# Kernel optimization log

Measured on AMD Instinct MI355X. Metric: run time of the kernel, lower is better.

## Reference

```python
import jax, jax.numpy as jnp
import numpy as np

B, C, D, H, W = 4, 128, 16, 16, 16
HID = 128
EPS = 1e-5


def setup_inputs() -> dict:
    key = jax.random.key(0)
    ks = jax.random.split(key, 10)
    s = 1.0 / np.sqrt(C)
    return {
        "x": jax.random.normal(ks[0], (B, C, D, H, W), dtype=jnp.float32),
        "Wq": jax.random.normal(ks[1], (HID, C), dtype=jnp.float32) * s,
        "bq": jax.random.normal(ks[2], (HID,), dtype=jnp.float32) * s,
        "Wk": jax.random.normal(ks[3], (HID, C), dtype=jnp.float32) * s,
        "bk": jax.random.normal(ks[4], (HID,), dtype=jnp.float32) * s,
        "Wv": jax.random.normal(ks[5], (HID, C), dtype=jnp.float32) * s,
        "bv": jax.random.normal(ks[6], (HID,), dtype=jnp.float32) * s,
        "bn_weight": jax.random.normal(ks[7], (HID,), dtype=jnp.float32),
        "bn_bias": jax.random.normal(ks[8], (HID,), dtype=jnp.float32),
        "gamma": jax.random.normal(ks[9], (1,), dtype=jnp.float32),
    }


def reference(x, Wq, bq, Wk, bk, Wv, bv, bn_weight, bn_bias, gamma):
    b, c, d, h, w = x.shape
    n = d * h * w
    xf = x.reshape(b, c, n)  # [B, C, N]
    # 1x1 conv3d == per-voxel linear: [B, hid, N]
    q = jnp.einsum("hc,bcn->bnh", Wq, xf) + bq  # [B, N, hid] (query permuted)
    k = jnp.einsum("hc,bcn->bhn", Wk, xf) + bk[None, :, None]  # [B, hid, N]
    v = jnp.einsum("hc,bcn->bhn", Wv, xf) + bv[None, :, None]  # [B, hid, N]
    # unscaled attention scores [B, N, N], softmax over last dim
    attn = jax.nn.softmax(jnp.einsum("bih,bhj->bij", q, k), axis=-1)
    # out[b,h,i] = sum_j v[b,h,j] * attn[b,i,j]
    out = jnp.einsum("bhj,bij->bhi", v, attn)  # [B, hid, N]
    # BatchNorm3d (training mode): per-channel stats over (B, N), biased var
    mean = jnp.mean(out, axis=(0, 2), keepdims=True)
    var = jnp.mean(jnp.square(out - mean), axis=(0, 2), keepdims=True)
    out = (out - mean) * jax.lax.rsqrt(var + EPS)
    out = out * bn_weight[None, :, None] + bn_bias[None, :, None]
    out = gamma[0] * out.reshape(b, c, d, h, w) + x
    return out
```

## Files before the change

### kernel.cpp

```cpp
#include <hip/hip_runtime.h>


#define NV 4096
#define LOG2E 1.44269504088896340736f
#define EPSV 1e-5f

typedef float f32x4 __attribute__((ext_vector_type(4)));
typedef short bf16x8 __attribute__((ext_vector_type(8)));
typedef unsigned short u16x4 __attribute__((ext_vector_type(4)));
typedef unsigned short u16x8 __attribute__((ext_vector_type(8)));
typedef unsigned int u32x2 __attribute__((ext_vector_type(2)));

static __device__ __forceinline__ unsigned short f2bf(float f) {
    union { float f; unsigned u; } v; v.f = f;
    unsigned r = v.u + 0x7FFFu + ((v.u >> 16) & 1u);
    return (unsigned short)(r >> 16);
}
static __device__ __forceinline__ float bf2f(unsigned short u) {
    union { unsigned u; float f; } v; v.u = ((unsigned)u) << 16; return v.f;
}
static __device__ __forceinline__ unsigned fbits(float f) {
    union { float f; unsigned u; } v; v.f = f; return v.u;
}

__global__ __launch_bounds__(256) void projx_kernel(
    const float* __restrict__ x,
    const float* __restrict__ Wq, const float* __restrict__ Wk,
    const float* __restrict__ Wv,
    const float* __restrict__ bq, const float* __restrict__ bk,
    const float* __restrict__ bv,
    unsigned short* __restrict__ Qb, unsigned short* __restrict__ Kb,
    unsigned short* __restrict__ Vb)
{
    __shared__ unsigned short xt[64 * 136];
    __shared__ unsigned short Wl[128 * 136];
    const int bid = blockIdx.x;
    const int m = bid >> 8, b = (bid >> 6) & 3, n0 = (bid & 63) << 6;
    const int t = threadIdx.x, w = t >> 6, lane = t & 63;
    const int quad = lane >> 4, l16 = lane & 15;

    const float* Wm = (m == 0) ? Wq : ((m == 1) ? Wk : Wv);
    const float* bias = (m == 0) ? bq : ((m == 1) ? bk : bv);

    #pragma unroll
    for (int it = 0; it < 32; ++it) {
        const int e = it * 256 + t;
        const int c = e >> 6, il = e & 63;
        xt[il * 136 + c] = f2bf(x[(((b << 7) + c) << 12) + n0 + il]);
    }
    #pragma unroll
    for (int it = 0; it < 16; ++it) {
        const int idx = it * 1024 + (t << 2);
        const float4 wv4 = *(const float4*)(Wm + idx);
        const int h = idx >> 7, c = idx & 127;
        u16x4 pk;
        pk[0] = f2bf(wv4.x); pk[1] = f2bf(wv4.y);
        pk[2] = f2bf(wv4.z); pk[3] = f2bf(wv4.w);
        *(u16x4*)(Wl + h * 136 + c) = pk;
    }
    __syncthreads();

    bf16x8 af[4];
    {
        const int il = (w << 4) + l16;
        #pragma unroll
        for (int ck = 0; ck < 4; ++ck)
            af[ck] = *(const bf16x8*)(xt + il * 136 + (ck << 5) + (quad << 3));
    }
    if (m == 2) __syncthreads();

    #pragma unroll
    for (int s = 0; s < 8; ++s) {
        const int h = (s << 4) + l16;
        f32x4 acc = {0.f, 0.f, 0.f, 0.f};
        #pragma unroll
        for (int ck = 0; ck < 4; ++ck) {
            const bf16x8 wf = *(const bf16x8*)(Wl + h * 136 + (ck << 5) + (quad << 3));
            acc = __builtin_amdgcn_mfma_f32_16x16x32_bf16(af[ck], wf, acc, 0, 0, 0);
        }
        const float bval = bias[h];
        if (m == 2) {
            #pragma unroll
            for (int r = 0; r < 4; ++r)
                xt[h * 66 + (w << 4) + (quad << 2) + r] = f2bf(acc[r] + bval);
        } else {
            #pragma unroll
            for (int r = 0; r < 4; ++r) {
                float val = acc[r] + bval;
                if (m == 0) val *= LOG2E;
                xt[((w << 4) + (quad << 2) + r) * 136 + h] = f2bf(val);
            }
        }
    }
    __syncthreads();
    if (m == 2) {
        #pragma unroll
        for (int it = 0; it < 32; ++it) {
            const int e = it * 256 + t;
            const int h = e >> 6, il = e & 63;
            Vb[(((b << 7) + h) << 12) + n0 + il] = xt[h * 66 + il];
        }
    } else {
        unsigned short* dst = (m == 0) ? Qb : Kb;
        #pragma unroll
        for (int it = 0; it < 4; ++it) {
            const int e = (it << 8) + t;
            const int row = e >> 4, c8 = (e & 15) << 3;
            *(bf16x8*)(dst + (((b << 12) + n0 + row) << 7) + c8) =
                *(const bf16x8*)(xt + row * 136 + c8);
        }
    }
}

template<int NSL>
__global__ __launch_bounds__(256, 2) void flash_kernel(
    const unsigned short* __restrict__ Qb,
    const unsigned short* __restrict__ Kb,
    const unsigned short* __restrict__ Vb,
    unsigned short* __restrict__ Opart, float* __restrict__ lpart,
    unsigned short* __restrict__ Obuf)
{
    __shared__ unsigned short Kt[64 * 128];
    __shared__ unsigned short Vt[128 * 64];
    __shared__ unsigned short pA[4][32 * 72];
    constexpr int NB = (NSL == 6) ? 768 : NSL * 128;
    const int bid = ((blockIdx.x & 7) * (NB >> 3)) + (blockIdx.x >> 3);
    const int sl = bid >> 7, b = (bid >> 5) & 3, ic = bid & 31;
    const int t = threadIdx.x, w = t >> 6, lane = t & 63;
    const int quad = lane >> 4, l16 = lane & 15;
    const int iw = (ic << 7) + (w << 5);

    int T, joff;
    if constexpr (NSL == 6) {
        T = 11 - (sl >= 4);
        joff = sl * 11 - ((sl >= 5) ? 1 : 0);
    } else {
        T = (NV / NSL) >> 6;
        joff = sl * T;
    }
    const int jbase = joff << 6;
    unsigned short* pAw = pA[w];

    const int ktg = t & 15, ktj = t >> 4;
    const int vtg = t & 7,  vth = t >> 3;
    const int kswz = (ktg ^ ktj) << 3;
    const int vswz = (vtg ^ (vth & 7)) << 3;

    bf16x8 qf[2][4];
    #pragma unroll
    for (int half = 0; half < 2; ++half) {
        const unsigned short* qp =
            Qb + (((b << 12) + iw + (half << 4) + l16) << 7) + (quad << 3);
        #pragma unroll
        for (int ck = 0; ck < 4; ++ck) qf[half][ck] = *(const bf16x8*)(qp + (ck << 5));
    }
    f32x4 Oacc[2][8];
    #pragma unroll
    for (int half = 0; half < 2; ++half)
        #pragma unroll
        for (int s = 0; s < 8; ++s) Oacc[half][s] = (f32x4){0.f, 0.f, 0.f, 0.f};
    float lsum0 = 0.f, lsum1 = 0.f;

    const unsigned short* Kbb = Kb + ((long)b << 19);
    const unsigned short* Vbb = Vb + ((long)b << 19);

    bf16x8 sk[4], sv[4];
    #pragma unroll
    for (int r = 0; r < 4; ++r)
        sk[r] = *(const bf16x8*)(Kbb + ((jbase + (r << 4) + ktj) << 7) + (ktg << 3));
    #pragma unroll
    for (int r = 0; r < 4; ++r)
        sv[r] = *(const bf16x8*)(Vbb + (((r << 5) + vth) << 12) + jbase + (vtg << 3));

    for (int t8 = 0; t8 < T; ++t8) {
        const int j0 = jbase + (t8 << 6);

        __syncthreads();
        #pragma unroll
        for (int r = 0; r < 4; ++r)
            *(bf16x8*)(Kt + (((r << 4) + ktj) << 7) + kswz) = sk[r];
        #pragma unroll
        for (int r = 0; r < 4; ++r)
            *(bf16x8*)(Vt + (((r << 5) + vth) << 6) + vswz) = sv[r];
        __syncthreads();

        if (t8 + 1 < T) {
            const int j1 = j0 + 64;
            #pragma unroll
            for (int r = 0; r < 4; ++r)
                sk[r] = *(const bf16x8*)(Kbb + ((j1 + (r << 4) + ktj) << 7) + (ktg << 3));
            #pragma unroll
            for (int r = 0; r < 4; ++r)
                sv[r] = *(const bf16x8*)(Vbb + (((r << 5) + vth) << 12) + j1 + (vtg << 3));
        }

        #pragma unroll
        for (int js = 0; js < 4; ++js) {
            bf16x8 kf[4];
            const int krow = ((js << 4) + l16) << 7;
            #pragma unroll
            for (int ck = 0; ck < 4; ++ck)
                kf[ck] = *(const bf16x8*)(Kt + krow + ((((ck << 2) + quad) ^ l16) << 3));
            f32x4 a0 = {0.f, 0.f, 0.f, 0.f}, a1 = {0.f, 0.f, 0.f, 0.f};
            __builtin_amdgcn_s_setprio(1);
            #pragma unroll
            for (int ck = 0; ck < 4; ++ck) {
                a0 = __builtin_amdgcn_mfma_f32_16x16x32_bf16(kf[ck], qf[0][ck], a0, 0, 0, 0);
                a1 = __builtin_amdgcn_mfma_f32_16x16x32_bf16(kf[ck], qf[1][ck], a1, 0, 0, 0);
            }
            __builtin_amdgcn_s_setprio(0);
            f32x4 e0, e1;
            #pragma unroll
            for (int r = 0; r < 4; ++r) {
                e0[r] = __builtin_amdgcn_exp2f(a0[r]);
                e1[r] = __builtin_amdgcn_exp2f(a1[r]);
            }
            lsum0 += (e0[0] + e0[1]) + (e0[2] + e0[3]);
            lsum1 += (e1[0] + e1[1]) + (e1[2] + e1[3]);
            u32x2 pk0, pk1;
            pk0[0] = __builtin_amdgcn_perm(fbits(e0[1]), fbits(e0[0]), 0x07060302u);
            pk0[1] = __builtin_amdgcn_perm(fbits(e0[3]), fbits(e0[2]), 0x07060302u);
            pk1[0] = __builtin_amdgcn_perm(fbits(e1[1]), fbits(e1[0]), 0x07060302u);
            pk1[1] = __builtin_amdgcn_perm(fbits(e1[3]), fbits(e1[2]), 0x07060302u);
            const int jc = (js << 4) + (quad << 2);
            *(u32x2*)(pAw + l16 * 72 + jc)        = pk0;
            *(u32x2*)(pAw + (16 + l16) * 72 + jc) = pk1;
        }
        bf16x8 pf[2][2];
        #pragma unroll
        for (int half = 0; half < 2; ++half)
            #pragma unroll
            for (int kh = 0; kh < 2; ++kh)
                pf[half][kh] = *(const bf16x8*)(pAw + ((half << 4) + l16) * 72 +
                                                (kh << 5) + (quad << 3));
        #pragma unroll
        for (int s = 0; s < 8; ++s) {
            const int vrow = ((s << 4) + l16) << 6;
            const bf16x8 v0 = *(const bf16x8*)(Vt + vrow + ((quad ^ (l16 & 7)) << 3));
            const bf16x8 v1 = *(const bf16x8*)(Vt + vrow + (((4 + quad) ^ (l16 & 7)) << 3));
            __builtin_amdgcn_s_setprio(1);
            Oacc[0][s] = __builtin_amdgcn_mfma_f32_16x16x32_bf16(v0, pf[0][0], Oacc[0][s], 0, 0, 0);
            Oacc[0][s] = __builtin_amdgcn_mfma_f32_16x16x32_bf16(v1, pf[0][1], Oacc[0][s], 0, 0, 0);
            Oacc[1][s] = __builtin_amdgcn_mfma_f32_16x16x32_bf16(v0, pf[1][0], Oacc[1][s], 0, 0, 0);
            Oacc[1][s] = __builtin_amdgcn_mfma_f32_16x16x32_bf16(v1, pf[1][1], Oacc[1][s], 0, 0, 0);
            __builtin_amdgcn_s_setprio(0);
        }
    }

    float l0 = lsum0; l0 += __shfl_xor(l0, 16); l0 += __shfl_xor(l0, 32);
    float l1 = lsum1; l1 += __shfl_xor(l1, 16); l1 += __shfl_xor(l1, 32);

    if (NSL == 1) {
        const float rl0 = 1.f / l0, rl1 = 1.f / l1;
        #pragma unroll
        for (int s = 0; s < 8; ++s)
            #pragma unroll
            for (int r = 0; r < 4; ++r) {
                const int h = (s << 4) + (quad << 2) + r;
                Obuf[(((b << 7) + h) << 12) + iw + l16]      = f2bf(Oacc[0][s][r] * rl0);
                Obuf[(((b << 7) + h) << 12) + iw + 16 + l16] = f2bf(Oacc[1][s][r] * rl1);
            }
    } else {
        const int slb = (sl << 2) + b;
        if (quad == 0) {
            lpart[(slb << 12) + iw + l16]      = l0;
            lpart[(slb << 12) + iw + 16 + l16] = l1;
        }
        unsigned short* Ob = Opart + ((long)slb << 19);
        #pragma unroll
        for (int half = 0; half < 2; ++half)
            #pragma unroll
            for (int s = 0; s < 8; ++s)
                #pragma unroll
                for (int r = 0; r < 4; ++r) {
                    const int h = (s << 4) + (quad << 2) + r;
                    Ob[(h << 12) + iw + (half << 4) + l16] = f2bf(Oacc[half][s][r]);
                }
    }
}

template<int NSL>
__global__ __launch_bounds__(1024) void mf_kernel(
    const unsigned short* __restrict__ Opart, const float* __restrict__ lpart,
    const float* __restrict__ x, const float* __restrict__ bnw,
    const float* __restrict__ bnb, const float* __restrict__ gammap,
    float* __restrict__ out)
{
    const int h = blockIdx.x;
    const int t = threadIdx.x;
    const int b = t >> 8;
    const int i0 = (t & 255) << 4;

    float A[16], L[16];
    #pragma unroll
    for (int k = 0; k < 16; ++k) { A[k] = 0.f; L[k] = 0.f; }
    #pragma unroll
    for (int sl = 0; sl < NSL; ++sl) {
        const int slb = (sl << 2) + b;
        const u16x8 u0 = *(const u16x8*)(Opart + ((long)slb << 19) + ((long)h << 12) + i0);
        const u16x8 u1 = *(const u16x8*)(Opart + ((long)slb << 19) + ((long)h << 12) + i0 + 8);
        const float* lp = lpart + (slb << 12) + i0;
        #pragma unroll
        for (int k = 0; k < 8; ++k) { A[k] += bf2f(u0[k]); A[8 + k] += bf2f(u1[k]); }
        #pragma unroll
        for (int k = 0; k < 4; ++k) {
            const float4 lv = *(const float4*)(lp + (k << 2));
            L[(k << 2) + 0] += lv.x; L[(k << 2) + 1] += lv.y;
            L[(k << 2) + 2] += lv.z; L[(k << 2) + 3] += lv.w;
        }
    }
    float o[16], s = 0.f, ss = 0.f;
    #pragma unroll
    for (int k = 0; k < 16; ++k) {
        o[k] = A[k] / L[k];
        s += o[k]; ss += o[k] * o[k];
    }
    #pragma unroll
    for (int off = 32; off; off >>= 1) {
        s  += __shfl_down(s, off);
        ss += __shfl_down(ss, off);
    }
    __shared__ float rs[16], rss[16], fin[2];
    const int wid = t >> 6;
    if ((t & 63) == 0) { rs[wid] = s; rss[wid] = ss; }
    __syncthreads();
    if (t == 0) {
        float s2 = 0.f, ss2 = 0.f;
        #pragma unroll
        for (int k = 0; k < 16; ++k) { s2 += rs[k]; ss2 += rss[k]; }
        fin[0] = s2; fin[1] = ss2;
    }
    __syncthreads();
    const float inv = 1.f / 16384.f;
    const float mean = fin[0] * inv;
    const float var  = fin[1] * inv - mean * mean;
    const float g = gammap[0];
    const float scale = bnw[h] * rsqrtf(var + EPSV);
    const float a  = g * scale;
    const float bb = g * (bnb[h] - mean * scale);

    const float* xp = x + (((b << 7) + h) << 12) + i0;
    float* op = out + (((b << 7) + h) << 12) + i0;
    #pragma unroll
    for (int k = 0; k < 4; ++k) {
        const float4 xv = *(const float4*)(xp + (k << 2));
        float4 r;
        r.x = o[(k << 2) + 0] * a + bb + xv.x;
        r.y = o[(k << 2) + 1] * a + bb + xv.y;
        r.z = o[(k << 2) + 2] * a + bb + xv.z;
        r.w = o[(k << 2) + 3] * a + bb + xv.w;
        *(float4*)(op + (k << 2)) = r;
    }
}

__global__ __launch_bounds__(1024) void mf1_kernel(
    const unsigned short* __restrict__ Obuf,
    const float* __restrict__ x, const float* __restrict__ bnw,
    const float* __restrict__ bnb, const float* __restrict__ gammap,
    float* __restrict__ out)
{
    const int h = blockIdx.x;
    const int t = threadIdx.x;
    const int b = t >> 8;
    const int i0 = (t & 255) << 4;
    const u16x8 u0 = *(const u16x8*)(Obuf + (((b << 7) + h) << 12) + i0);
    const u16x8 u1 = *(const u16x8*)(Obuf + (((b << 7) + h) << 12) + i0 + 8);
    float o[16], s = 0.f, ss = 0.f;
    #pragma unroll
    for (int k = 0; k < 8; ++k) { o[k] = bf2f(u0[k]); o[8 + k] = bf2f(u1[k]); }
    #pragma unroll
    for (int k = 0; k < 16; ++k) { s += o[k]; ss += o[k] * o[k]; }
    #pragma unroll
    for (int off = 32; off; off >>= 1) {
        s  += __shfl_down(s, off);
        ss += __shfl_down(ss, off);
    }
    __shared__ float rs[16], rss[16], fin[2];
    const int wid = t >> 6;
    if ((t & 63) == 0) { rs[wid] = s; rss[wid] = ss; }
    __syncthreads();
    if (t == 0) {
        float s2 = 0.f, ss2 = 0.f;
        #pragma unroll
        for (int k = 0; k < 16; ++k) { s2 += rs[k]; ss2 += rss[k]; }
        fin[0] = s2; fin[1] = ss2;
    }
    __syncthreads();
    const float inv = 1.f / 16384.f;
    const float mean = fin[0] * inv;
    const float var  = fin[1] * inv - mean * mean;
    const float g = gammap[0];
    const float scale = bnw[h] * rsqrtf(var + EPSV);
    const float a  = g * scale;
    const float bb = g * (bnb[h] - mean * scale);
    const float* xp = x + (((b << 7) + h) << 12) + i0;
    float* op = out + (((b << 7) + h) << 12) + i0;
    #pragma unroll
    for (int k = 0; k < 4; ++k) {
        const float4 xv = *(const float4*)(xp + (k << 2));
        float4 r;
        r.x = o[(k << 2) + 0] * a + bb + xv.x;
        r.y = o[(k << 2) + 1] * a + bb + xv.y;
        r.z = o[(k << 2) + 2] * a + bb + xv.z;
        r.w = o[(k << 2) + 3] * a + bb + xv.w;
        *(float4*)(op + (k << 2)) = r;
    }
}

extern "C" void kernel_launch(void* const* d_in, const int* in_sizes, int n_in,
                              void* d_out, int out_size, void* d_ws, size_t ws_size,
                              hipStream_t stream) {
    const float* x   = (const float*)d_in[0];
    const float* Wq  = (const float*)d_in[1];
    const float* bq  = (const float*)d_in[2];
    const float* Wk  = (const float*)d_in[3];
    const float* bk  = (const float*)d_in[4];
    const float* Wv  = (const float*)d_in[5];
    const float* bv  = (const float*)d_in[6];
    const float* bnw = (const float*)d_in[7];
    const float* bnb = (const float*)d_in[8];
    const float* gam = (const float*)d_in[9];
    float* out = (float*)d_out;

    char* ws = (char*)d_ws;
    unsigned short* Obuf = (unsigned short*)(ws);
    unsigned short* Qb   = (unsigned short*)(ws + (4u  << 20));
    unsigned short* Kb   = (unsigned short*)(ws + (8u  << 20));
    unsigned short* Vb   = (unsigned short*)(ws + (12u << 20));
    float*          lpart = (float*)(ws + (16u << 20) + (128u << 10));
    unsigned short* Opart = (unsigned short*)(ws + (17u << 20));

    int nsl = 1;
    if      (ws_size >= (17ull << 20) + (32ull << 20)) nsl = 6;
    else if (ws_size >= (17ull << 20) + (16ull << 20)) nsl = 4;
    else if (ws_size >= (17ull << 20) + (8ull  << 20)) nsl = 2;

    projx_kernel<<<768, 256, 0, stream>>>(x, Wq, Wk, Wv, bq, bk, bv, Qb, Kb, Vb);
    if (nsl == 6) {
        flash_kernel<6><<<768, 256, 0, stream>>>(Qb, Kb, Vb, Opart, lpart, Obuf);
        mf_kernel<6><<<128, 1024, 0, stream>>>(Opart, lpart, x, bnw, bnb, gam, out);
    } else if (nsl == 4) {
        flash_kernel<4><<<512, 256, 0, stream>>>(Qb, Kb, Vb, Opart, lpart, Obuf);
        mf_kernel<4><<<128, 1024, 0, stream>>>(Opart, lpart, x, bnw, bnb, gam, out);
    } else if (nsl == 2) {
        flash_kernel<2><<<256, 256, 0, stream>>>(Qb, Kb, Vb, Opart, lpart, Obuf);
        mf_kernel<2><<<128, 1024, 0, stream>>>(Opart, lpart, x, bnw, bnb, gam, out);
    } else {
        flash_kernel<1><<<128, 256, 0, stream>>>(Qb, Kb, Vb, Opart, lpart, Obuf);
        mf1_kernel<<<128, 1024, 0, stream>>>(Obuf, x, bnw, bnb, gam, out);
    }
}
```

Before: 148.3 us.

## Double-buffer K in LDS, stream V fragments from global, vectorize x loads

The flash kernel now double-buffers the K tile in shared memory, so each iteration needs one barrier instead of two. V no longer goes through LDS: each wave reads its MFMA operand fragments directly from global memory with a two-step register prefetch. The setprio hints are removed. The projection kernel loads x with float4 instead of scalar loads. The aim is to cut LDS traffic and barrier stalls, at the cost of redundant global/L2 reads of V across the four waves and more exposed load latency in the PV loop.

```diff
diff --git a/kernel.cpp b/kernel.cpp
--- a/kernel.cpp
+++ b/kernel.cpp
@@ -43,10 +43,14 @@
     const float* bias = (m == 0) ? bq : ((m == 1) ? bk : bv);
 
     #pragma unroll
-    for (int it = 0; it < 32; ++it) {
-        const int e = it * 256 + t;
-        const int c = e >> 6, il = e & 63;
-        xt[il * 136 + c] = f2bf(x[(((b << 7) + c) << 12) + n0 + il]);
+    for (int it = 0; it < 8; ++it) {
+        const int e = (it << 8) + t;
+        const int c = e >> 4, i4 = (e & 15) << 2;
+        const float4 xv = *(const float4*)(x + (((b << 7) + c) << 12) + n0 + i4);
+        xt[(i4 + 0) * 136 + c] = f2bf(xv.x);
+        xt[(i4 + 1) * 136 + c] = f2bf(xv.y);
+        xt[(i4 + 2) * 136 + c] = f2bf(xv.z);
+        xt[(i4 + 3) * 136 + c] = f2bf(xv.w);
     }
     #pragma unroll
     for (int it = 0; it < 16; ++it) {
@@ -120,8 +124,7 @@
     unsigned short* __restrict__ Opart, float* __restrict__ lpart,
     unsigned short* __restrict__ Obuf)
 {
-    __shared__ unsigned short Kt[64 * 128];
-    __shared__ unsigned short Vt[128 * 64];
+    __shared__ unsigned short Kt[2][64 * 128];
     __shared__ unsigned short pA[4][32 * 72];
     constexpr int NB = (NSL == 6) ? 768 : NSL * 128;
     const int bid = ((blockIdx.x & 7) * (NB >> 3)) + (blockIdx.x >> 3);
@@ -142,9 +145,7 @@
     unsigned short* pAw = pA[w];
 
     const int ktg = t & 15, ktj = t >> 4;
-    const int vtg = t & 7,  vth = t >> 3;
     const int kswz = (ktg ^ ktj) << 3;
-    const int vswz = (vtg ^ (vth & 7)) << 3;
 
     bf16x8 qf[2][4];
     #pragma unroll
@@ -163,35 +164,32 @@
 
     const unsigned short* Kbb = Kb + ((long)b << 19);
     const unsigned short* Vbb = Vb + ((long)b << 19);
-
-    bf16x8 sk[4], sv[4];
+    const int vcol = quad << 3;
+
+    bf16x8 sk[4];
     #pragma unroll
     for (int r = 0; r < 4; ++r)
         sk[r] = *(const bf16x8*)(Kbb + ((jbase + (r << 4) + ktj) << 7) + (ktg << 3));
     #pragma unroll
     for (int r = 0; r < 4; ++r)
-        sv[r] = *(const bf16x8*)(Vbb + (((r << 5) + vth) << 12) + jbase + (vtg << 3));
+        *(bf16x8*)(Kt[0] + (((r << 4) + ktj) << 7) + kswz) = sk[r];
+    __syncthreads();
 
     for (int t8 = 0; t8 < T; ++t8) {
         const int j0 = jbase + (t8 << 6);
-
-        __syncthreads();
-        #pragma unroll
-        for (int r = 0; r < 4; ++r)
-            *(bf16x8*)(Kt + (((r << 4) + ktj) << 7) + kswz) = sk[r];
-        #pragma unroll
-        for (int r = 0; r < 4; ++r)
-            *(bf16x8*)(Vt + (((r << 5) + vth) << 6) + vswz) = sv[r];
-        __syncthreads();
+        const unsigned short* Ktc = Kt[t8 & 1];
+        unsigned short* Ktn = Kt[(t8 & 1) ^ 1];
+
+        bf16x8 vc0 = *(const bf16x8*)(Vbb + (l16 << 12) + j0 + vcol);
+        bf16x8 vc1 = *(const bf16x8*)(Vbb + (l16 << 12) + j0 + vcol + 32);
+        bf16x8 vn0 = *(const bf16x8*)(Vbb + ((16 + l16) << 12) + j0 + vcol);
+        bf16x8 vn1 = *(const bf16x8*)(Vbb + ((16 + l16) << 12) + j0 + vcol + 32);
 
         if (t8 + 1 < T) {
             const int j1 = j0 + 64;
             #pragma unroll
             for (int r = 0; r < 4; ++r)
                 sk[r] = *(const bf16x8*)(Kbb + ((j1 + (r << 4) + ktj) << 7) + (ktg << 3));
-            #pragma unroll
-            for (int r = 0; r < 4; ++r)
-                sv[r] = *(const bf16x8*)(Vbb + (((r << 5) + vth) << 12) + j1 + (vtg << 3));
         }
 
         #pragma unroll
@@ -200,15 +198,13 @@
             const int krow = ((js << 4) + l16) << 7;
             #pragma unroll
             for (int ck = 0; ck < 4; ++ck)
-                kf[ck] = *(const bf16x8*)(Kt + krow + ((((ck << 2) + quad) ^ l16) << 3));
+                kf[ck] = *(const bf16x8*)(Ktc + krow + ((((ck << 2) + quad) ^ l16) << 3));
             f32x4 a0 = {0.f, 0.f, 0.f, 0.f}, a1 = {0.f, 0.f, 0.f, 0.f};
-            __builtin_amdgcn_s_setprio(1);
             #pragma unroll
             for (int ck = 0; ck < 4; ++ck) {
                 a0 = __builtin_amdgcn_mfma_f32_16x16x32_bf16(kf[ck], qf[0][ck], a0, 0, 0, 0);
                 a1 = __builtin_amdgcn_mfma_f32_16x16x32_bf16(kf[ck], qf[1][ck], a1, 0, 0, 0);
             }
-            __builtin_amdgcn_s_setprio(0);
             f32x4 e0, e1;
             #pragma unroll
             for (int r = 0; r < 4; ++r) {
@@ -235,15 +231,23 @@
                                                 (kh << 5) + (quad << 3));
         #pragma unroll
         for (int s = 0; s < 8; ++s) {
-            const int vrow = ((s << 4) + l16) << 6;
-            const bf16x8 v0 = *(const bf16x8*)(Vt + vrow + ((quad ^ (l16 & 7)) << 3));
-            const bf16x8 v1 = *(const bf16x8*)(Vt + vrow + (((4 + quad) ^ (l16 & 7)) << 3));
-            __builtin_amdgcn_s_setprio(1);
+            const bf16x8 v0 = vc0, v1 = vc1;
+            vc0 = vn0; vc1 = vn1;
+            if (s < 6) {
+                vn0 = *(const bf16x8*)(Vbb + ((((s + 2) << 4) + l16) << 12) + j0 + vcol);
+                vn1 = *(const bf16x8*)(Vbb + ((((s + 2) << 4) + l16) << 12) + j0 + vcol + 32);
+            }
             Oacc[0][s] = __builtin_amdgcn_mfma_f32_16x16x32_bf16(v0, pf[0][0], Oacc[0][s], 0, 0, 0);
             Oacc[0][s] = __builtin_amdgcn_mfma_f32_16x16x32_bf16(v1, pf[0][1], Oacc[0][s], 0, 0, 0);
             Oacc[1][s] = __builtin_amdgcn_mfma_f32_16x16x32_bf16(v0, pf[1][0], Oacc[1][s], 0, 0, 0);
             Oacc[1][s] = __builtin_amdgcn_mfma_f32_16x16x32_bf16(v1, pf[1][1], Oacc[1][s], 0, 0, 0);
-            __builtin_amdgcn_s_setprio(0);
+        }
+
+        if (t8 + 1 < T) {
+            #pragma unroll
+            for (int r = 0; r < 4; ++r)
+                *(bf16x8*)(Ktn + (((r << 4) + ktj) << 7) + kswz) = sk[r];
+            __syncthreads();
         }
     }
 
```

Result: slower. 195.0 us (+31.4%).
